# Kernel tuning notes

Hardware: AMD Instinct MI355X
Metric: run time of the kernel (lower is better)

Reference implementation:

```python
import jax, jax.numpy as jnp
import numpy as np

N, E = 20000, 100000
IN_CH, HID_CH, EDGE_DIM, NUM_CLASSES = 32, 32, 16, 10


def setup_inputs() -> dict:
    key = jax.random.key(0)
    ks = jax.random.split(key, 20)
    s = 0.05
    inp = {
        "x": jax.random.normal(ks[0], (N, IN_CH), jnp.float32),
        "edge_index": jax.random.randint(ks[1], (2, E), 0, N, jnp.int64),
        "edge_attr": jax.random.normal(ks[2], (E, EDGE_DIM), jnp.float32),
        # edge MLP 1: edge_dim -> in*hid -> in*hid (weights stored as (in, out))
        "e1_w1": jax.random.normal(ks[3], (EDGE_DIM, IN_CH * HID_CH), jnp.float32) * s,
        "e1_b1": jnp.zeros((IN_CH * HID_CH,), jnp.float32),
        "e1_w2": jax.random.normal(ks[4], (IN_CH * HID_CH, IN_CH * HID_CH), jnp.float32) * s,
        "e1_b2": jnp.zeros((IN_CH * HID_CH,), jnp.float32),
        "root1": jax.random.normal(ks[5], (IN_CH, HID_CH), jnp.float32) * s,
        "bias1": jnp.zeros((HID_CH,), jnp.float32),
        # edge MLP 2: edge_dim -> hid*hid -> hid*hid
        "e2_w1": jax.random.normal(ks[6], (EDGE_DIM, HID_CH * HID_CH), jnp.float32) * s,
        "e2_b1": jnp.zeros((HID_CH * HID_CH,), jnp.float32),
        "e2_w2": jax.random.normal(ks[7], (HID_CH * HID_CH, HID_CH * HID_CH), jnp.float32) * s,
        "e2_b2": jnp.zeros((HID_CH * HID_CH,), jnp.float32),
        "root2": jax.random.normal(ks[8], (HID_CH, HID_CH), jnp.float32) * s,
        "bias2": jnp.zeros((HID_CH,), jnp.float32),
        "lin_w": jax.random.normal(ks[9], (HID_CH, NUM_CLASSES), jnp.float32) * s,
        "lin_b": jnp.zeros((NUM_CLASSES,), jnp.float32),
    }
    return inp


def _nnconv_mean(x, src, dst, edge_attr, w1, b1, w2, b2, root, bias, in_ch, out_ch, n_nodes):
    # edge MLP -> per-edge weight matrix [E, in_ch, out_ch]
    h = jax.nn.relu(edge_attr @ w1 + b1) @ w2 + b2
    W = h.reshape(-1, in_ch, out_ch)
    # message: x_j @ W_e (gather source features, per-edge matmul)
    msg = jnp.einsum('ei,eio->eo', x[src], W)
    # scatter-mean to target nodes
    agg = jax.ops.segment_sum(msg, dst, num_segments=n_nodes)
    cnt = jax.ops.segment_sum(jnp.ones((msg.shape[0],), msg.dtype), dst, num_segments=n_nodes)
    mean = agg / jnp.maximum(cnt, 1.0)[:, None]
    return mean + x @ root + bias


def reference(x, edge_index, edge_attr,
              e1_w1, e1_b1, e1_w2, e1_b2, root1, bias1,
              e2_w1, e2_b1, e2_w2, e2_b2, root2, bias2,
              lin_w, lin_b):
    src, dst = edge_index[0], edge_index[1]
    n = x.shape[0]
    h = jax.nn.relu(_nnconv_mean(x, src, dst, edge_attr, e1_w1, e1_b1, e1_w2, e1_b2,
                                 root1, bias1, IN_CH, HID_CH, n))
    # dropout p=0.5 is identity in eval mode
    h = jax.nn.relu(_nnconv_mean(h, src, dst, edge_attr, e2_w1, e2_b1, e2_w2, e2_b2,
                                 root2, bias2, HID_CH, HID_CH, n))
    return h @ lin_w + lin_b
```

## Files before the change

kernel.cpp:

```cpp
#include <hip/hip_runtime.h>

typedef __attribute__((ext_vector_type(8))) short sh8;
typedef __attribute__((ext_vector_type(4))) float f32x4;

#define E_EDGES 100000
#define E_PAD   100096
#define N_NODES 20000

__device__ __forceinline__ unsigned short f2bf(float f) {
  union { float f; unsigned int u; } v; v.f = f;
  unsigned int r = v.u + 0x7FFFu + ((v.u >> 16) & 1u);
  return (unsigned short)(r >> 16);
}

__device__ __forceinline__ void async16(const void* g, void* l) {
  __builtin_amdgcn_global_load_lds((const __attribute__((address_space(1))) unsigned int*)g,
                                   (__attribute__((address_space(3))) unsigned int*)l,
                                   16, 0, 0);
}

__global__ void transpose_w2_kernel(const float* __restrict__ w2, unsigned short* __restrict__ w2t) {
  __shared__ float tile[32][33];
  int b = blockIdx.x;
  int bx = b & 31, by = b >> 5;
  int lx = threadIdx.x & 31, ly = threadIdx.x >> 5;
#pragma unroll
  for (int j = 0; j < 4; ++j)
    tile[ly + j*8][lx] = w2[(by*32 + ly + j*8)*1024 + bx*32 + lx];
  __syncthreads();
#pragma unroll
  for (int j = 0; j < 4; ++j)
    w2t[(size_t)(bx*32 + ly + j*8)*1024 + by*32 + lx] = f2bf(tile[lx][ly + j*8]);
}

__global__ __launch_bounds__(256)
void edge_mlp1_kernel(const float* __restrict__ ea, const float* __restrict__ w1,
                      const float* __restrict__ b1, unsigned short* __restrict__ h1) {
  __shared__ float eas[8][16];
  const int tid = threadIdx.x;
  const int e0 = blockIdx.x * 8;
  if (tid < 128) {
    int g = tid >> 4, d = tid & 15;
    int ge = e0 + g;
    eas[g][d] = (ge < E_EDGES) ? ea[(size_t)ge*16 + d] : 0.f;
  }
  __syncthreads();
  const int c0 = tid * 4;
  float4 bb = *(const float4*)(b1 + c0);
  float4 acc[8];
#pragma unroll
  for (int g = 0; g < 8; ++g) acc[g] = bb;
#pragma unroll
  for (int d = 0; d < 16; ++d) {
    float4 w = *(const float4*)(w1 + (size_t)d*1024 + c0);
#pragma unroll
    for (int g = 0; g < 8; ++g) {
      float ev = eas[g][d];
      acc[g].x += ev*w.x; acc[g].y += ev*w.y; acc[g].z += ev*w.z; acc[g].w += ev*w.w;
    }
  }
#pragma unroll
  for (int g = 0; g < 8; ++g) {
    ushort4 o;
    if (e0 + g < E_EDGES) {
      o.x = f2bf(fmaxf(acc[g].x, 0.f)); o.y = f2bf(fmaxf(acc[g].y, 0.f));
      o.z = f2bf(fmaxf(acc[g].z, 0.f)); o.w = f2bf(fmaxf(acc[g].w, 0.f));
    } else {
      o.x = o.y = o.z = o.w = 0;
    }
    *(ushort4*)(h1 + (size_t)(e0 + g)*1024 + c0) = o;
  }
}

__global__ void count_kernel(const int* __restrict__ dst, float* __restrict__ cnt) {
  int t = blockIdx.x*256 + threadIdx.x;
  if (t < E_EDGES) atomicAdd(&cnt[dst[t]], 1.0f);
}

__global__ __launch_bounds__(256, 4)
void gemm_scatter_kernel(const unsigned short* __restrict__ h1,
                         const unsigned short* __restrict__ w2t,
                         const float* __restrict__ b2,
                         const float* __restrict__ xin,
                         const int* __restrict__ src,
                         const int* __restrict__ dst,
                         float* __restrict__ agg) {
  __shared__ __align__(16) unsigned char smem[32768];
  unsigned short* Als = (unsigned short*)smem;
  unsigned short* Bls = (unsigned short*)(smem + 16384);
  float* msgbuf = (float*)smem;
  __shared__ __align__(16) float xg[128][4];
  __shared__ int dsts[128];

  const int tid  = threadIdx.x;
  const int wave = tid >> 6, lane = tid & 63;
  const int wm = wave >> 1, wn = wave & 1;
  const int lr = lane >> 4, lc = lane & 15;
  const int logical = (blockIdx.x & 7) * 782 + (blockIdx.x >> 3);
  const int tile_m = logical >> 3, tile_n = logical & 7;
  const int e0 = tile_m * 128, n0 = tile_n * 128;

  if (tid < 128) {
    int ge = e0 + tid;
    float4 v = make_float4(0.f, 0.f, 0.f, 0.f);
    if (ge < E_EDGES) {
      int s = src[ge];
      v = *(const float4*)(xin + (size_t)s*32 + tile_n*4);
    }
    *(float4*)xg[tid] = v;
  } else {
    int e = tid - 128;
    int ge = e0 + e;
    dsts[e] = (ge < E_EDGES) ? dst[ge] : -1;
  }

  f32x4 acc[4][4];
#pragma unroll
  for (int i = 0; i < 4; ++i)
#pragma unroll
    for (int j = 0; j < 4; ++j) acc[i][j] = (f32x4){0.f,0.f,0.f,0.f};

  const unsigned short* Ag = h1  + (size_t)e0*1024;
  const unsigned short* Bg = w2t + (size_t)n0*1024;
  const int rj     = lane >> 3;
  const int srow   = wave*32 + rj;
  const int scol   = 8*((lane & 7) ^ rj);
  const int swzb   = (lc & 7) << 4;

  for (int kt = 0; kt < 16; ++kt) {
    const int k0 = kt * 64;
    __syncthreads();
#pragma unroll
    for (int j = 0; j < 4; ++j) {
      async16(Ag + (size_t)(srow + j*8)*1024 + k0 + scol, &Als[wave*2048 + j*512]);
      async16(Bg + (size_t)(srow + j*8)*1024 + k0 + scol, &Bls[wave*2048 + j*512]);
    }
    __syncthreads();
#pragma unroll
    for (int kk = 0; kk < 2; ++kk) {
      sh8 av[4], bv[4];
#pragma unroll
      for (int mi = 0; mi < 4; ++mi)
        av[mi] = *(const sh8*)((const char*)Als + (wm*64 + mi*16 + lc)*128 + ((kk*64 + lr*16) ^ swzb));
#pragma unroll
      for (int ni = 0; ni < 4; ++ni)
        bv[ni] = *(const sh8*)((const char*)Bls + (wn*64 + ni*16 + lc)*128 + ((kk*64 + lr*16) ^ swzb));
#pragma unroll
      for (int mi = 0; mi < 4; ++mi)
#pragma unroll
        for (int ni = 0; ni < 4; ++ni)
          acc[mi][ni] = __builtin_amdgcn_mfma_f32_16x16x32_bf16(av[mi], bv[ni], acc[mi][ni], 0, 0, 0);
    }
  }

  float b2c[4];
#pragma unroll
  for (int ni = 0; ni < 4; ++ni) b2c[ni] = b2[n0 + wn*64 + ni*16 + lc];

  float ms0[4][4], ms1[4][4];
#pragma unroll
  for (int mi = 0; mi < 4; ++mi)
#pragma unroll
    for (int r = 0; r < 4; ++r) {
      int e = wm*64 + mi*16 + lr*4 + r;
      float x0 = xg[e][2*wn], x1 = xg[e][2*wn + 1];
      ms0[mi][r] = (acc[mi][0][r] + b2c[0])*x0 + (acc[mi][2][r] + b2c[2])*x1;
      ms1[mi][r] = (acc[mi][1][r] + b2c[1])*x0 + (acc[mi][3][r] + b2c[3])*x1;
    }

  __syncthreads();
  if (wn == 0) {
#pragma unroll
    for (int mi = 0; mi < 4; ++mi)
#pragma unroll
      for (int r = 0; r < 4; ++r) {
        int e = wm*64 + mi*16 + lr*4 + r;
        msgbuf[e*33 + lc]      = ms0[mi][r];
        msgbuf[e*33 + lc + 16] = ms1[mi][r];
      }
  }
  __syncthreads();
  if (wn == 1) {
#pragma unroll
    for (int mi = 0; mi < 4; ++mi)
#pragma unroll
      for (int r = 0; r < 4; ++r) {
        int e = wm*64 + mi*16 + lr*4 + r;
        msgbuf[e*33 + lc]      += ms0[mi][r];
        msgbuf[e*33 + lc + 16] += ms1[mi][r];
      }
  }
  __syncthreads();
  for (int t = tid; t < 128*32; t += 256) {
    int e = t >> 5, o = t & 31;
    int dn = dsts[e];
    if (dn >= 0) atomicAdd(&agg[(size_t)dn*32 + o], msgbuf[e*33 + o]);
  }
}

__global__ void node_update_kernel(const float* __restrict__ agg, const float* __restrict__ cnt,
                                   const float* __restrict__ xin, const float* __restrict__ root,
                                   const float* __restrict__ bias, float* __restrict__ outp) {
  int t = blockIdx.x*256 + threadIdx.x;
  if (t >= N_NODES*32) return;
  int n = t >> 5, i = t & 31;
  const float* xr = xin + (size_t)n*32;
  float s = bias[i];
#pragma unroll
  for (int j = 0; j < 32; ++j) s += xr[j]*root[j*32 + i];
  float c = cnt[n]; c = c > 1.f ? c : 1.f;
  float v = agg[t]/c + s;
  outp[t] = fmaxf(v, 0.f);
}

__global__ void final_linear_kernel(const float* __restrict__ h, const float* __restrict__ lw,
                                    const float* __restrict__ lb, float* __restrict__ out) {
  int t = blockIdx.x*256 + threadIdx.x;
  if (t >= N_NODES*10) return;
  int n = t / 10, k = t % 10;
  const float* hr = h + (size_t)n*32;
  float s = lb[k];
#pragma unroll
  for (int i = 0; i < 32; ++i) s += hr[i]*lw[i*10 + k];
  out[t] = s;
}

extern "C" void kernel_launch(void* const* d_in, const int* in_sizes, int n_in,
                              void* d_out, int out_size, void* d_ws, size_t ws_size,
                              hipStream_t stream) {
  const float* x     = (const float*)d_in[0];
  const int*   ei    = (const int*)d_in[1];
  const float* ea    = (const float*)d_in[2];
  const float* e1w1  = (const float*)d_in[3];
  const float* e1b1  = (const float*)d_in[4];
  const float* e1w2  = (const float*)d_in[5];
  const float* e1b2  = (const float*)d_in[6];
  const float* root1 = (const float*)d_in[7];
  const float* bias1 = (const float*)d_in[8];
  const float* e2w1  = (const float*)d_in[9];
  const float* e2b1  = (const float*)d_in[10];
  const float* e2w2  = (const float*)d_in[11];
  const float* e2b2  = (const float*)d_in[12];
  const float* root2 = (const float*)d_in[13];
  const float* bias2 = (const float*)d_in[14];
  const float* linw  = (const float*)d_in[15];
  const float* linb  = (const float*)d_in[16];
  const int* srcp = ei;
  const int* dstp = ei + E_EDGES;

  char* ws = (char*)d_ws;
  size_t off = 0;
  auto alloc = [&](size_t bytes) { void* p = ws + off; off += (bytes + 255) & ~(size_t)255; return p; };
  unsigned short* h1buf = (unsigned short*)alloc((size_t)E_PAD*1024*2);
  unsigned short* w2t   = (unsigned short*)alloc((size_t)1024*1024*2);
  float* agg  = (float*)alloc((size_t)N_NODES*32*4);
  float* cnt  = (float*)alloc((size_t)N_NODES*4);
  float* out1 = (float*)alloc((size_t)N_NODES*32*4);
  float* hbuf = (float*)alloc((size_t)N_NODES*32*4);
  (void)ws_size; (void)n_in; (void)in_sizes; (void)out_size;

  hipMemsetAsync(agg, 0, (size_t)N_NODES*32*4, stream);
  hipMemsetAsync(cnt, 0, (size_t)N_NODES*4, stream);
  count_kernel<<<(E_EDGES + 255)/256, 256, 0, stream>>>(dstp, cnt);

  transpose_w2_kernel<<<1024, 256, 0, stream>>>(e1w2, w2t);
  edge_mlp1_kernel<<<E_PAD/8, 256, 0, stream>>>(ea, e1w1, e1b1, h1buf);
  gemm_scatter_kernel<<<(E_PAD/128)*8, 256, 0, stream>>>(h1buf, w2t, e1b2, x, srcp, dstp, agg);
  node_update_kernel<<<(N_NODES*32 + 255)/256, 256, 0, stream>>>(agg, cnt, x, root1, bias1, out1);

  hipMemsetAsync(agg, 0, (size_t)N_NODES*32*4, stream);
  transpose_w2_kernel<<<1024, 256, 0, stream>>>(e2w2, w2t);
  edge_mlp1_kernel<<<E_PAD/8, 256, 0, stream>>>(ea, e2w1, e2b1, h1buf);
  gemm_scatter_kernel<<<(E_PAD/128)*8, 256, 0, stream>>>(h1buf, w2t, e2b2, out1, srcp, dstp, agg);
  node_update_kernel<<<(N_NODES*32 + 255)/256, 256, 0, stream>>>(agg, cnt, out1, root2, bias2, hbuf);

  final_linear_kernel<<<(N_NODES*10 + 255)/256, 256, 0, stream>>>(hbuf, linw, linb, (float*)d_out);
}
```

Measured before the change: 639.7 us.

## Double-buffer GEMM LDS tiles and widen edge MLP blocks to 16 edges

The GEMM-scatter kernel now double-buffers its A and B tiles in 64 KB of LDS. It issues the async global-to-LDS loads for the next K tile before running the MFMAs on the current one, and drops one of the two barriers per iteration. This is meant to hide load latency behind compute. In exchange, launch bounds fall from 4 to 2 blocks per CU and LDS use doubles, which lowers occupancy. Separately, the first edge MLP kernel processes 16 edges per block instead of 8, so each weight load is reused across more edges, at the cost of more registers.

```diff
diff --git a/kernel.cpp b/kernel.cpp
--- a/kernel.cpp
+++ b/kernel.cpp
@@ -36,10 +36,10 @@
 __global__ __launch_bounds__(256)
 void edge_mlp1_kernel(const float* __restrict__ ea, const float* __restrict__ w1,
                       const float* __restrict__ b1, unsigned short* __restrict__ h1) {
-  __shared__ float eas[8][16];
+  __shared__ float eas[16][16];
   const int tid = threadIdx.x;
-  const int e0 = blockIdx.x * 8;
-  if (tid < 128) {
+  const int e0 = blockIdx.x * 16;
+  {
     int g = tid >> 4, d = tid & 15;
     int ge = e0 + g;
     eas[g][d] = (ge < E_EDGES) ? ea[(size_t)ge*16 + d] : 0.f;
@@ -47,20 +47,20 @@
   __syncthreads();
   const int c0 = tid * 4;
   float4 bb = *(const float4*)(b1 + c0);
-  float4 acc[8];
-#pragma unroll
-  for (int g = 0; g < 8; ++g) acc[g] = bb;
+  float4 acc[16];
+#pragma unroll
+  for (int g = 0; g < 16; ++g) acc[g] = bb;
 #pragma unroll
   for (int d = 0; d < 16; ++d) {
     float4 w = *(const float4*)(w1 + (size_t)d*1024 + c0);
 #pragma unroll
-    for (int g = 0; g < 8; ++g) {
+    for (int g = 0; g < 16; ++g) {
       float ev = eas[g][d];
       acc[g].x += ev*w.x; acc[g].y += ev*w.y; acc[g].z += ev*w.z; acc[g].w += ev*w.w;
     }
   }
 #pragma unroll
-  for (int g = 0; g < 8; ++g) {
+  for (int g = 0; g < 16; ++g) {
     ushort4 o;
     if (e0 + g < E_EDGES) {
       o.x = f2bf(fmaxf(acc[g].x, 0.f)); o.y = f2bf(fmaxf(acc[g].y, 0.f));
@@ -77,7 +77,7 @@
   if (t < E_EDGES) atomicAdd(&cnt[dst[t]], 1.0f);
 }
 
-__global__ __launch_bounds__(256, 4)
+__global__ __launch_bounds__(256, 2)
 void gemm_scatter_kernel(const unsigned short* __restrict__ h1,
                          const unsigned short* __restrict__ w2t,
                          const float* __restrict__ b2,
@@ -85,9 +85,7 @@
                          const int* __restrict__ src,
                          const int* __restrict__ dst,
                          float* __restrict__ agg) {
-  __shared__ __align__(16) unsigned char smem[32768];
-  unsigned short* Als = (unsigned short*)smem;
-  unsigned short* Bls = (unsigned short*)(smem + 16384);
+  __shared__ __align__(16) unsigned char smem[65536];
   float* msgbuf = (float*)smem;
   __shared__ __align__(16) float xg[128][4];
   __shared__ int dsts[128];
@@ -127,31 +125,44 @@
   const int scol   = 8*((lane & 7) ^ rj);
   const int swzb   = (lc & 7) << 4;
 
+#define ABUF(b) (smem + (b)*16384)
+#define BBUF(b) (smem + 32768 + (b)*16384)
+#define STAGE(b, kt) do { _Pragma("unroll")                                     \
+    for (int j = 0; j < 4; ++j) {                                               \
+      async16(Ag + (size_t)(srow + j*8)*1024 + (kt)*64 + scol,                  \
+              ABUF(b) + wave*4096 + j*1024);                                    \
+      async16(Bg + (size_t)(srow + j*8)*1024 + (kt)*64 + scol,                  \
+              BBUF(b) + wave*4096 + j*1024);                                    \
+    } } while (0)
+
+  STAGE(0, 0);
+  __syncthreads();
+
   for (int kt = 0; kt < 16; ++kt) {
-    const int k0 = kt * 64;
-    __syncthreads();
-#pragma unroll
-    for (int j = 0; j < 4; ++j) {
-      async16(Ag + (size_t)(srow + j*8)*1024 + k0 + scol, &Als[wave*2048 + j*512]);
-      async16(Bg + (size_t)(srow + j*8)*1024 + k0 + scol, &Bls[wave*2048 + j*512]);
-    }
-    __syncthreads();
+    const int cur = kt & 1;
+    if (kt + 1 < 16) STAGE(cur ^ 1, kt + 1);
+    const char* Ab = (const char*)ABUF(cur);
+    const char* Bb = (const char*)BBUF(cur);
 #pragma unroll
     for (int kk = 0; kk < 2; ++kk) {
       sh8 av[4], bv[4];
 #pragma unroll
       for (int mi = 0; mi < 4; ++mi)
-        av[mi] = *(const sh8*)((const char*)Als + (wm*64 + mi*16 + lc)*128 + ((kk*64 + lr*16) ^ swzb));
+        av[mi] = *(const sh8*)(Ab + (wm*64 + mi*16 + lc)*128 + ((kk*64 + lr*16) ^ swzb));
 #pragma unroll
       for (int ni = 0; ni < 4; ++ni)
-        bv[ni] = *(const sh8*)((const char*)Bls + (wn*64 + ni*16 + lc)*128 + ((kk*64 + lr*16) ^ swzb));
+        bv[ni] = *(const sh8*)(Bb + (wn*64 + ni*16 + lc)*128 + ((kk*64 + lr*16) ^ swzb));
 #pragma unroll
       for (int mi = 0; mi < 4; ++mi)
 #pragma unroll
         for (int ni = 0; ni < 4; ++ni)
           acc[mi][ni] = __builtin_amdgcn_mfma_f32_16x16x32_bf16(av[mi], bv[ni], acc[mi][ni], 0, 0, 0);
     }
-  }
+    __syncthreads();
+  }
+#undef STAGE
+#undef ABUF
+#undef BBUF
 
   float b2c[4];
 #pragma unroll
@@ -264,13 +275,13 @@
   count_kernel<<<(E_EDGES + 255)/256, 256, 0, stream>>>(dstp, cnt);
 
   transpose_w2_kernel<<<1024, 256, 0, stream>>>(e1w2, w2t);
-  edge_mlp1_kernel<<<E_PAD/8, 256, 0, stream>>>(ea, e1w1, e1b1, h1buf);
+  edge_mlp1_kernel<<<E_PAD/16, 256, 0, stream>>>(ea, e1w1, e1b1, h1buf);
   gemm_scatter_kernel<<<(E_PAD/128)*8, 256, 0, stream>>>(h1buf, w2t, e1b2, x, srcp, dstp, agg);
   node_update_kernel<<<(N_NODES*32 + 255)/256, 256, 0, stream>>>(agg, cnt, x, root1, bias1, out1);
 
   hipMemsetAsync(agg, 0, (size_t)N_NODES*32*4, stream);
   transpose_w2_kernel<<<1024, 256, 0, stream>>>(e2w2, w2t);
-  edge_mlp1_kernel<<<E_PAD/8, 256, 0, stream>>>(ea, e2w1, e2b1, h1buf);
+  edge_mlp1_kernel<<<E_PAD/16, 256, 0, stream>>>(ea, e2w1, e2b1, h1buf);
   gemm_scatter_kernel<<<(E_PAD/128)*8, 256, 0, stream>>>(h1buf, w2t, e2b2, out1, srcp, dstp, agg);
   node_update_kernel<<<(N_NODES*32 + 255)/256, 256, 0, stream>>>(agg, cnt, out1, root2, bias2, hbuf);
 
```

Result: slower. 860.1 us (+34.5%).

## Pre-pack W2 into MFMA fragment layout and read B directly from global

Applied to the files above, without the earlier changes.

The transpose kernel now writes W2 in bf16 in a blocked layout that matches the MFMA B-fragment order, so the GEMM kernel loads B operands straight from global/L2 instead of staging them through LDS. This cuts LDS usage from 32KB to about 20KB, which could allow higher occupancy, and removes the B async copies. Separately, the edge MLP1 kernel handles 16 edges per block instead of 8, reusing each W1 load across more edges. The trade-off is that B loads now go through global memory latency on every k-step with no prefetch, and the edge kernel needs more registers.

```diff
diff --git a/kernel.cpp b/kernel.cpp
--- a/kernel.cpp
+++ b/kernel.cpp
@@ -19,27 +19,31 @@
                                    16, 0, 0);
 }
 
-__global__ void transpose_w2_kernel(const float* __restrict__ w2, unsigned short* __restrict__ w2t) {
+__global__ void transpose_w2_kernel(const float* __restrict__ w2, unsigned short* __restrict__ w2b) {
   __shared__ float tile[32][33];
   int b = blockIdx.x;
   int bx = b & 31, by = b >> 5;
   int lx = threadIdx.x & 31, ly = threadIdx.x >> 5;
 #pragma unroll
   for (int j = 0; j < 4; ++j)
-    tile[ly + j*8][lx] = w2[(by*32 + ly + j*8)*1024 + bx*32 + lx];
-  __syncthreads();
-#pragma unroll
-  for (int j = 0; j < 4; ++j)
-    w2t[(size_t)(bx*32 + ly + j*8)*1024 + by*32 + lx] = f2bf(tile[lx][ly + j*8]);
+    tile[ly + j*8][lx] = w2[(size_t)(by*32 + ly + j*8)*1024 + bx*32 + lx];
+  __syncthreads();
+#pragma unroll
+  for (int j = 0; j < 4; ++j) {
+    int n = bx*32 + ly + j*8;
+    int k = by*32 + lx;
+    size_t idx = ((size_t)(n >> 4)*128 + (k >> 3))*128 + (n & 15)*8 + (k & 7);
+    w2b[idx] = f2bf(tile[lx][ly + j*8]);
+  }
 }
 
 __global__ __launch_bounds__(256)
 void edge_mlp1_kernel(const float* __restrict__ ea, const float* __restrict__ w1,
                       const float* __restrict__ b1, unsigned short* __restrict__ h1) {
-  __shared__ float eas[8][16];
+  __shared__ float eas[16][16];
   const int tid = threadIdx.x;
-  const int e0 = blockIdx.x * 8;
-  if (tid < 128) {
+  const int e0 = blockIdx.x * 16;
+  {
     int g = tid >> 4, d = tid & 15;
     int ge = e0 + g;
     eas[g][d] = (ge < E_EDGES) ? ea[(size_t)ge*16 + d] : 0.f;
@@ -47,20 +51,20 @@
   __syncthreads();
   const int c0 = tid * 4;
   float4 bb = *(const float4*)(b1 + c0);
-  float4 acc[8];
-#pragma unroll
-  for (int g = 0; g < 8; ++g) acc[g] = bb;
+  float4 acc[16];
+#pragma unroll
+  for (int g = 0; g < 16; ++g) acc[g] = bb;
 #pragma unroll
   for (int d = 0; d < 16; ++d) {
     float4 w = *(const float4*)(w1 + (size_t)d*1024 + c0);
 #pragma unroll
-    for (int g = 0; g < 8; ++g) {
+    for (int g = 0; g < 16; ++g) {
       float ev = eas[g][d];
       acc[g].x += ev*w.x; acc[g].y += ev*w.y; acc[g].z += ev*w.z; acc[g].w += ev*w.w;
     }
   }
 #pragma unroll
-  for (int g = 0; g < 8; ++g) {
+  for (int g = 0; g < 16; ++g) {
     ushort4 o;
     if (e0 + g < E_EDGES) {
       o.x = f2bf(fmaxf(acc[g].x, 0.f)); o.y = f2bf(fmaxf(acc[g].y, 0.f));
@@ -79,18 +83,17 @@
 
 __global__ __launch_bounds__(256, 4)
 void gemm_scatter_kernel(const unsigned short* __restrict__ h1,
-                         const unsigned short* __restrict__ w2t,
+                         const unsigned short* __restrict__ w2b,
                          const float* __restrict__ b2,
                          const float* __restrict__ xin,
                          const int* __restrict__ src,
                          const int* __restrict__ dst,
                          float* __restrict__ agg) {
-  __shared__ __align__(16) unsigned char smem[32768];
+  __shared__ __align__(16) unsigned char smem[19968];
   unsigned short* Als = (unsigned short*)smem;
-  unsigned short* Bls = (unsigned short*)(smem + 16384);
   float* msgbuf = (float*)smem;
-  __shared__ __align__(16) float xg[128][4];
-  __shared__ int dsts[128];
+  float (*xg)[4] = (float (*)[4])(smem + 17408);
+  int* dsts = (int*)(smem + 19456);
 
   const int tid  = threadIdx.x;
   const int wave = tid >> 6, lane = tid & 63;
@@ -120,31 +123,30 @@
 #pragma unroll
     for (int j = 0; j < 4; ++j) acc[i][j] = (f32x4){0.f,0.f,0.f,0.f};
 
-  const unsigned short* Ag = h1  + (size_t)e0*1024;
-  const unsigned short* Bg = w2t + (size_t)n0*1024;
+  const unsigned short* Ag = h1 + (size_t)e0*1024;
   const int rj     = lane >> 3;
   const int srow   = wave*32 + rj;
   const int scol   = 8*((lane & 7) ^ rj);
   const int swzb   = (lc & 7) << 4;
 
+  const char* Bb = (const char*)w2b
+                 + (size_t)(tile_n*8 + wn*4)*32768 + lr*256 + lc*16;
+
   for (int kt = 0; kt < 16; ++kt) {
-    const int k0 = kt * 64;
     __syncthreads();
 #pragma unroll
-    for (int j = 0; j < 4; ++j) {
-      async16(Ag + (size_t)(srow + j*8)*1024 + k0 + scol, &Als[wave*2048 + j*512]);
-      async16(Bg + (size_t)(srow + j*8)*1024 + k0 + scol, &Bls[wave*2048 + j*512]);
-    }
+    for (int j = 0; j < 4; ++j)
+      async16(Ag + (size_t)(srow + j*8)*1024 + kt*64 + scol, &Als[wave*2048 + j*512]);
     __syncthreads();
 #pragma unroll
     for (int kk = 0; kk < 2; ++kk) {
       sh8 av[4], bv[4];
 #pragma unroll
+      for (int ni = 0; ni < 4; ++ni)
+        bv[ni] = *(const sh8*)(Bb + ni*32768 + kt*2048 + kk*1024);
+#pragma unroll
       for (int mi = 0; mi < 4; ++mi)
         av[mi] = *(const sh8*)((const char*)Als + (wm*64 + mi*16 + lc)*128 + ((kk*64 + lr*16) ^ swzb));
-#pragma unroll
-      for (int ni = 0; ni < 4; ++ni)
-        bv[ni] = *(const sh8*)((const char*)Bls + (wn*64 + ni*16 + lc)*128 + ((kk*64 + lr*16) ^ swzb));
 #pragma unroll
       for (int mi = 0; mi < 4; ++mi)
 #pragma unroll
@@ -252,7 +254,7 @@
   size_t off = 0;
   auto alloc = [&](size_t bytes) { void* p = ws + off; off += (bytes + 255) & ~(size_t)255; return p; };
   unsigned short* h1buf = (unsigned short*)alloc((size_t)E_PAD*1024*2);
-  unsigned short* w2t   = (unsigned short*)alloc((size_t)1024*1024*2);
+  unsigned short* w2b   = (unsigned short*)alloc((size_t)1024*1024*2);
   float* agg  = (float*)alloc((size_t)N_NODES*32*4);
   float* cnt  = (float*)alloc((size_t)N_NODES*4);
   float* out1 = (float*)alloc((size_t)N_NODES*32*4);
@@ -263,15 +265,15 @@
   hipMemsetAsync(cnt, 0, (size_t)N_NODES*4, stream);
   count_kernel<<<(E_EDGES + 255)/256, 256, 0, stream>>>(dstp, cnt);
 
-  transpose_w2_kernel<<<1024, 256, 0, stream>>>(e1w2, w2t);
-  edge_mlp1_kernel<<<E_PAD/8, 256, 0, stream>>>(ea, e1w1, e1b1, h1buf);
-  gemm_scatter_kernel<<<(E_PAD/128)*8, 256, 0, stream>>>(h1buf, w2t, e1b2, x, srcp, dstp, agg);
+  transpose_w2_kernel<<<1024, 256, 0, stream>>>(e1w2, w2b);
+  edge_mlp1_kernel<<<E_PAD/16, 256, 0, stream>>>(ea, e1w1, e1b1, h1buf);
+  gemm_scatter_kernel<<<(E_PAD/128)*8, 256, 0, stream>>>(h1buf, w2b, e1b2, x, srcp, dstp, agg);
   node_update_kernel<<<(N_NODES*32 + 255)/256, 256, 0, stream>>>(agg, cnt, x, root1, bias1, out1);
 
   hipMemsetAsync(agg, 0, (size_t)N_NODES*32*4, stream);
-  transpose_w2_kernel<<<1024, 256, 0, stream>>>(e2w2, w2t);
-  edge_mlp1_kernel<<<E_PAD/8, 256, 0, stream>>>(ea, e2w1, e2b1, h1buf);
-  gemm_scatter_kernel<<<(E_PAD/128)*8, 256, 0, stream>>>(h1buf, w2t, e2b2, out1, srcp, dstp, agg);
+  transpose_w2_kernel<<<1024, 256, 0, stream>>>(e2w2, w2b);
+  edge_mlp1_kernel<<<E_PAD/16, 256, 0, stream>>>(ea, e2w1, e2b1, h1buf);
+  gemm_scatter_kernel<<<(E_PAD/128)*8, 256, 0, stream>>>(h1buf, w2b, e2b2, out1, srcp, dstp, agg);
   node_update_kernel<<<(N_NODES*32 + 255)/256, 256, 0, stream>>>(agg, cnt, out1, root2, bias2, hbuf);
 
   final_linear_kernel<<<(N_NODES*10 + 255)/256, 256, 0, stream>>>(hbuf, linw, linb, (float*)d_out);
```

Measured after the change: 681.0 us. 1.06x slower.
